# Kernel optimization log

Hardware: AMD Instinct MI355X
Metric: run time of the kernel (lower is better)

## Reference

```python
import jax, jax.numpy as jnp
import numpy as np

D_MODEL = 1024
N_HEADS = 16
D_K = D_MODEL // N_HEADS


def _glorot(key, fan_in, fan_out):
    limit = np.sqrt(6.0 / (fan_in + fan_out)).astype(np.float32)
    return jax.random.uniform(key, (fan_in, fan_out), jnp.float32, -limit, limit)


def setup_inputs() -> dict:
    key = jax.random.key(0)
    kx, kq, kk, kv = jax.random.split(key, 4)
    x = jax.random.normal(kx, (2, 2048, D_MODEL), jnp.float32)
    Wq = _glorot(kq, D_MODEL, D_MODEL)
    Wk = _glorot(kk, D_MODEL, D_MODEL)
    Wv = _glorot(kv, D_MODEL, D_MODEL)
    bq = jnp.zeros((D_MODEL,), jnp.float32)
    bk = jnp.zeros((D_MODEL,), jnp.float32)
    bv = jnp.zeros((D_MODEL,), jnp.float32)
    return {"x": x, "Wq": Wq, "bq": bq, "Wk": Wk, "bk": bk, "Wv": Wv, "bv": bv}


def reference(x, Wq, bq, Wk, bk, Wv, bv):
    B, S, _ = x.shape
    # QKV projections (Dense layers with bias)
    q = (x @ Wq + bq).reshape(B, S, N_HEADS, D_K).transpose(0, 2, 1, 3)  # [B,H,S,Dk]
    k = (x @ Wk + bk).reshape(B, S, N_HEADS, D_K).transpose(0, 2, 1, 3)
    v = (x @ Wv + bv).reshape(B, S, N_HEADS, D_K).transpose(0, 2, 1, 3)
    # raw exp-based softmax (NO max subtraction, per original module)
    scores = jnp.einsum('bhqd,bhkd->bhqk', q, k) / np.sqrt(D_K).astype(np.float32)
    scores = jnp.exp(scores)
    attn = scores / (jnp.sum(scores, axis=-1, keepdims=True) + 1e-8)
    context = jnp.einsum('bhqk,bhkd->bhqd', attn, v)  # [B,H,S,Dk]
    return context.transpose(0, 2, 1, 3).reshape(B, S, N_HEADS * D_K)
```

## Files before the change

### kernel.cpp

```cpp
#include <hip/hip_runtime.h>
#include <hip/hip_bf16.h>
#include <stdint.h>

typedef __bf16 bf16x8 __attribute__((ext_vector_type(8)));
typedef __bf16 bf16x4 __attribute__((ext_vector_type(4)));
typedef float  f32x4  __attribute__((ext_vector_type(4)));
typedef short  s16x4  __attribute__((ext_vector_type(4)));
typedef short  s16x8  __attribute__((ext_vector_type(8)));
typedef unsigned short u16_t;

#define MFMA(a, b, c)   __builtin_amdgcn_mfma_f32_16x16x32_bf16((a), (b), (c), 0, 0, 0)

__device__ __forceinline__ bf16x8 cat8(s16x4 a, s16x4 b) {
  s16x8 t = __builtin_shufflevector(a, b, 0, 1, 2, 3, 4, 5, 6, 7);
  return *(bf16x8*)&t;
}
__device__ __forceinline__ bf16x8 b8(s16x8 v) {
  bf16x8 r; __builtin_memcpy(&r, &v, 16); return r;
}

__device__ __forceinline__ void cp16(const void* g, void* l) {
  __builtin_amdgcn_global_load_lds(
      (const __attribute__((address_space(1))) unsigned int*)g,
      (__attribute__((address_space(3))) unsigned int*)l, 16, 0, 0);
}

__global__ __launch_bounds__(256) void k_prep(const float* __restrict__ x,
                                              const float* __restrict__ W0,
                                              const float* __restrict__ W1,
                                              const float* __restrict__ W2,
                                              u16_t* __restrict__ xb,
                                              u16_t* __restrict__ Wt) {
  __shared__ u16_t T[64][65];
  int bx = blockIdx.x, t = threadIdx.x;
  if (bx < 4096) {
    int i = bx * 256 + t;
    float4 f = ((const float4*)x)[i];
    bf16x4 o = {(__bf16)f.x, (__bf16)f.y, (__bf16)f.z, (__bf16)f.w};
    *(bf16x4*)&xb[(size_t)i * 4] = o;
    return;
  }
  int j = bx - 4096;
  int nx = j & 15, ny = (j >> 4) & 15, z = j >> 8;
  const float* W = z == 0 ? W0 : (z == 1 ? W1 : W2);
  int k0 = ny * 64, n0 = nx * 64;
#pragma unroll
  for (int i = 0; i < 16; i++) {
    int e = i * 256 + t, r = e >> 6, c = e & 63;
    __bf16 hv = (__bf16)W[(size_t)(k0 + r) * 1024 + n0 + c];
    T[r][c] = *(u16_t*)&hv;
  }
  __syncthreads();
  size_t base = ((size_t)z * 1024 + n0) * 1024 + k0;
#pragma unroll
  for (int i = 0; i < 16; i++) {
    int e = i * 256 + t, r = e >> 6, c = e & 63;
    Wt[base + (size_t)r * 1024 + c] = T[c][r];
  }
}

__global__ __launch_bounds__(512, 2) void k_gemm_qkv(
    const u16_t* __restrict__ A, const u16_t* __restrict__ Bt,
    const float* __restrict__ bq, const float* __restrict__ bk,
    const float* __restrict__ bv,
    u16_t* __restrict__ Qo, u16_t* __restrict__ Ko, u16_t* __restrict__ Vo) {
  __shared__ u16_t smem[57344];
  u16_t* As = smem;
  u16_t* Bs = smem + 32768;

  const int tid = threadIdx.x, lane = tid & 63, wv = tid >> 6;
  const int quad = lane >> 4, col = lane & 15;
  const int wm = wv >> 2, wn = wv & 3;

  int bid = blockIdx.x;
  int wg = (bid & 7) * 32 + (bid >> 3);
  const int tn = (wg & 15) * 192, tm = (wg >> 4) << 8;

  const int r16 = lane >> 2, c4 = lane & 3;
  const int srow = wv * 16 + r16;
  const int skoff = ((c4 ^ ((r16 >> 1) & 3)) << 3);
  const int sdst = srow * 32 + (c4 << 3);
  const size_t gA0 = (size_t)(tm + srow) * 1024 + skoff;
  const size_t gB0 = (size_t)(tn + srow) * 1024 + skoff;

  f32x4 acc[8][3] = {};

#define STAGE(kt, h, b) do {                                     \
    int dA_ = (b) * 16384 + (h) * 8192 + sdst;                   \
    int dB_ = (b) * 12288 + (h) * 6144 + sdst;                   \
    size_t s_ = (size_t)(kt) * 64 + (h) * 32;                    \
    cp16(A + gA0 + s_, As + dA_);                                \
    cp16(A + gA0 + s_ + (size_t)128 * 1024, As + dA_ + 4096);    \
    cp16(Bt + gB0 + s_, Bs + dB_);                               \
    if (wv < 4)                                                  \
      cp16(Bt + gB0 + s_ + (size_t)128 * 1024, Bs + dB_ + 4096); \
  } while (0)

#define BAR()    asm volatile("s_barrier" ::: "memory")
#define WAITV(N) asm volatile("s_waitcnt vmcnt(" #N ")" ::: "memory")
#define WAITL()  asm volatile("s_waitcnt lgkmcnt(0)" ::: "memory")
#define SCHED0() __builtin_amdgcn_sched_barrier(0)

  STAGE(0, 0, 0);
  STAGE(0, 1, 0);
  WAITV(3);
  BAR();

  const int swz8 = (((lane >> 4) ^ ((col >> 1) & 3)) << 3);
  const int abase = (wm * 128 + col) * 32 + swz8;
  const int bbase = (wn * 48 + col) * 32 + swz8;

  for (int t = 0; t < 16; ++t) {
    const int cur = t & 1, nxt = cur ^ 1;
    const u16_t* Ap = As + cur * 16384;
    const u16_t* Bp = Bs + cur * 12288;
    bf16x8 af[4], bf[3];

#pragma unroll
    for (int i = 0; i < 4; i++) af[i] = *(const bf16x8*)&Ap[abase + i * 512];
#pragma unroll
    for (int j = 0; j < 3; j++) bf[j] = *(const bf16x8*)&Bp[bbase + j * 512];
    if (t + 1 < 16) STAGE(t + 1, 0, nxt);
    BAR(); WAITL(); SCHED0();
    __builtin_amdgcn_s_setprio(1);
#pragma unroll
    for (int i = 0; i < 4; i++)
#pragma unroll
      for (int j = 0; j < 3; j++) acc[i][j] = MFMA(af[i], bf[j], acc[i][j]);
    __builtin_amdgcn_s_setprio(0);
    BAR();

#pragma unroll
    for (int i = 0; i < 4; i++) af[i] = *(const bf16x8*)&Ap[abase + (i + 4) * 512];
    if (t + 1 < 16) { STAGE(t + 1, 1, nxt); WAITV(6); }
    else            { WAITV(0); }
    BAR(); WAITL(); SCHED0();
    __builtin_amdgcn_s_setprio(1);
#pragma unroll
    for (int i = 0; i < 4; i++)
#pragma unroll
      for (int j = 0; j < 3; j++) acc[i + 4][j] = MFMA(af[i], bf[j], acc[i + 4][j]);
    __builtin_amdgcn_s_setprio(0);
    BAR();

#pragma unroll
    for (int i = 0; i < 4; i++) af[i] = *(const bf16x8*)&Ap[8192 + abase + i * 512];
#pragma unroll
    for (int j = 0; j < 3; j++) bf[j] = *(const bf16x8*)&Bp[6144 + bbase + j * 512];
    BAR(); WAITL(); SCHED0();
    __builtin_amdgcn_s_setprio(1);
#pragma unroll
    for (int i = 0; i < 4; i++)
#pragma unroll
      for (int j = 0; j < 3; j++) acc[i][j] = MFMA(af[i], bf[j], acc[i][j]);
    __builtin_amdgcn_s_setprio(0);
    BAR();

#pragma unroll
    for (int i = 0; i < 4; i++) af[i] = *(const bf16x8*)&Ap[8192 + abase + (i + 4) * 512];
    if (t + 1 < 16) WAITV(3);
    WAITL();
    BAR(); SCHED0();
    __builtin_amdgcn_s_setprio(1);
#pragma unroll
    for (int i = 0; i < 4; i++)
#pragma unroll
      for (int j = 0; j < 3; j++) acc[i + 4][j] = MFMA(af[i], bf[j], acc[i + 4][j]);
    __builtin_amdgcn_s_setprio(0);
    BAR();
  }

#undef STAGE

#pragma unroll
  for (int nt = 0; nt < 3; nt++) {
    int gn = tn + wn * 48 + nt * 16 + col;
    int mat = gn >> 10, d = gn & 1023, h = d >> 6, dk = d & 63;
    const float* bias = mat == 0 ? bq : (mat == 1 ? bk : bv);
    float bb = bias[d];
    if (mat == 2) {
#pragma unroll
      for (int mt = 0; mt < 8; mt++) {
        int gm = tm + wm * 128 + mt * 16 + quad * 4;
        int b = gm >> 11, s = gm & 2047;
        bf16x4 pk4;
#pragma unroll
        for (int r = 0; r < 4; r++) pk4[r] = (__bf16)(acc[mt][nt][r] + bb);
        *(bf16x4*)&Vo[((size_t)((b * 16 + h) * 64 + dk)) * 2048 + s] = pk4;
      }
    } else {
      u16_t* O = mat == 0 ? Qo : Ko;
      const float scl = mat == 0 ? 0.18033688011112042f : 1.0f;
#pragma unroll
      for (int mt = 0; mt < 8; mt++) {
#pragma unroll
        for (int r = 0; r < 4; r++) {
          int gm = tm + wm * 128 + mt * 16 + quad * 4 + r;
          int b = gm >> 11, s = gm & 2047;
          __bf16 hv = (__bf16)((acc[mt][nt][r] + bb) * scl);
          O[((size_t)((b * 16 + h) * 2048 + s)) * 64 + dk] = *(u16_t*)&hv;
        }
      }
    }
  }
}

__global__ __launch_bounds__(256, 2) void k_attn(const u16_t* __restrict__ Q,
                                                 const u16_t* __restrict__ K,
                                                 const u16_t* __restrict__ Vt,
                                                 float* __restrict__ out) {
  __shared__ u16_t smem[24576];
  u16_t* Qs  = smem;
  u16_t* Ksb = smem + 8192;
  u16_t* Vsb = smem + 16384;
  const int tid = threadIdx.x, lane = tid & 63, wv = tid >> 6;
  const int quad = lane >> 4, col = lane & 15;

  const int bid = blockIdx.x;
  const int bh = (bid & 7) + 8 * ((bid >> 3) >> 4);
  const int qt = (bid >> 3) & 15;
  const int b = bh >> 4, h = bh & 15;
  const int r8 = lane >> 3, c8 = lane & 7;

  const u16_t* Qg = Q + ((size_t)bh * 2048 + qt * 128) * 64;
  const u16_t* Kg = K + (size_t)bh * 2048 * 64;
  const u16_t* Vg = Vt + (size_t)bh * 64 * 2048;

  const int lch  = c8 ^ r8;
  const int row0 = (wv * 2) * 8 + r8, row1 = (wv * 2 + 1) * 8 + r8;
  const int ldst0 = (wv * 2) * 512 + lane * 8;
  const int ldst1 = (wv * 2 + 1) * 512 + lane * 8;
  const int gk0 = row0 * 64 + lch * 8,   gk1 = row1 * 64 + lch * 8;
  const int gv0 = row0 * 2048 + lch * 8, gv1 = row1 * 2048 + lch * 8;

#pragma unroll
  for (int i = 0; i < 4; i++) {
    int c = wv * 4 + i;
    cp16(Qg + (c * 8 + r8) * 64 + lch * 8, Qs + c * 512 + lane * 8);
  }
  cp16(Kg + gk0, Ksb + ldst0);
  cp16(Kg + gk1, Ksb + ldst1);
  __syncthreads();

  bf16x8 qf[2][2];
#pragma unroll
  for (int nt = 0; nt < 2; nt++)
#pragma unroll
    for (int ks = 0; ks < 2; ks++) {
      int row = wv * 32 + nt * 16 + col;
      qf[nt][ks] = *(const bf16x8*)&Qs[row * 64 + (((ks * 4 + quad) ^ (row & 7)) * 8)];
    }

  int ka[2][4];
#pragma unroll
  for (int ks = 0; ks < 2; ks++)
#pragma unroll
    for (int mt = 0; mt < 4; mt++) {
      int row = mt * 16 + col;
      ka[ks][mt] = row * 64 + (((ks * 4 + quad) ^ (row & 7)) * 8);
    }
  int va0[2][4], va1[2][4];
#pragma unroll
  for (int g = 0; g < 2; g++)
#pragma unroll
    for (int dt = 0; dt < 4; dt++) {
      int row = dt * 16 + col;
      int cc = g * 4 + (quad >> 1);
      va0[g][dt] = row * 64 + ((cc ^ (row & 7)) * 8) + (quad & 1) * 4;
      va1[g][dt] = row * 64 + (((cc + 2) ^ (row & 7)) * 8) + (quad & 1) * 4;
    }

  const short one_bf = (short)0x3F80;
  s16x8 ones8s = {one_bf, one_bf, one_bf, one_bf, one_bf, one_bf, one_bf, one_bf};
  const bf16x8 ones8 = *(bf16x8*)&ones8s;
  const f32x4 z4 = {0.f, 0.f, 0.f, 0.f};

  f32x4 ao[2][4] = {};
  f32x4 dn[2] = {};
  s16x8 pA[2][2] = {}, pB[2][2] = {};

#define ATTN_STEP(KT, CUR, PFW, PFR, DO_PV, DO_PRE) do {                              \
    const u16_t* Kc = Ksb + (CUR) * 4096;                                             \
    const u16_t* Vp = Vsb + ((CUR) ^ 1) * 4096;                                       \
    u16_t* Kn = Ksb + ((CUR) ^ 1) * 4096;                                             \
    u16_t* Vn = Vsb + (CUR) * 4096;                                                   \
    if (DO_PRE) {                                                                     \
      const u16_t* kb = Kg + (size_t)((KT) + 1) * 4096;                               \
      cp16(kb + gk0, Kn + ldst0);                                                     \
      cp16(kb + gk1, Kn + ldst1);                                                     \
    }                                                                                 \
    {                                                                                 \
      const u16_t* vb = Vg + (size_t)(KT) * 64;                                       \
      cp16(vb + gv0, Vn + ldst0);                                                     \
      cp16(vb + gv1, Vn + ldst1);                                                     \
    }                                                                                 \
    f32x4 sc[4][2];                                                                   \
    __builtin_amdgcn_s_setprio(1);                                                    \
    _Pragma("unroll")                                                                 \
    for (int ks = 0; ks < 2; ks++) {                                                  \
      bf16x8 kf[4];                                                                   \
      _Pragma("unroll")                                                               \
      for (int mt = 0; mt < 4; mt++) kf[mt] = *(const bf16x8*)&Kc[ka[ks][mt]];        \
      _Pragma("unroll")                                                               \
      for (int mt = 0; mt < 4; mt++)                                                  \
        _Pragma("unroll")                                                             \
        for (int nt = 0; nt < 2; nt++)                                                \
          sc[mt][nt] = ks ? MFMA(kf[mt], qf[nt][1], sc[mt][nt])                       \
                          : MFMA(kf[mt], qf[nt][0], z4);                              \
    }                                                                                 \
    if (DO_PV) {                                                                      \
      bf16x8 pa00 = b8(PFR[0][0]), pa01 = b8(PFR[0][1]);                              \
      bf16x8 pa10 = b8(PFR[1][0]), pa11 = b8(PFR[1][1]);                              \
      _Pragma("unroll")                                                               \
      for (int dt = 0; dt < 4; dt++) {                                                \
        bf16x8 vv0 = cat8(*(const s16x4*)&Vp[va0[0][dt]],                             \
                          *(const s16x4*)&Vp[va1[0][dt]]);                            \
        bf16x8 vv1 = cat8(*(const s16x4*)&Vp[va0[1][dt]],                             \
                          *(const s16x4*)&Vp[va1[1][dt]]);                            \
        ao[0][dt] = MFMA(pa00, vv0, ao[0][dt]);                                       \
        ao[0][dt] = MFMA(pa01, vv1, ao[0][dt]);                                       \
        ao[1][dt] = MFMA(pa10, vv0, ao[1][dt]);                                       \
        ao[1][dt] = MFMA(pa11, vv1, ao[1][dt]);                                       \
      }                                                                               \
    }                                                                                 \
    __builtin_amdgcn_s_setprio(0);                                                    \
    _Pragma("unroll")                                                                 \
    for (int mt = 0; mt < 4; mt++)                                                    \
      _Pragma("unroll")                                                               \
      for (int nt = 0; nt < 2; nt++)                                                  \
        _Pragma("unroll")                                                             \
        for (int r = 0; r < 4; r++) {                                                 \
          __bf16 e = (__bf16)__builtin_amdgcn_exp2f(sc[mt][nt][r]);                   \
          PFW[nt][mt >> 1][(mt & 1) * 4 + r] = *(short*)&e;                           \
        }                                                                             \
    dn[0] = MFMA(b8(PFW[0][0]), ones8, dn[0]);                                        \
    dn[0] = MFMA(b8(PFW[0][1]), ones8, dn[0]);                                        \
    dn[1] = MFMA(b8(PFW[1][0]), ones8, dn[1]);                                        \
    dn[1] = MFMA(b8(PFW[1][1]), ones8, dn[1]);                                        \
    __syncthreads();                                                                  \
  } while (0)

  ATTN_STEP(0, 0, pA, pB, 0, 1);
  ATTN_STEP(1, 1, pB, pA, 1, 1);
#pragma unroll 1
  for (int kt2 = 1; kt2 < 15; kt2++) {
    int kt0 = kt2 * 2;
    ATTN_STEP(kt0,     0, pA, pB, 1, 1);
    ATTN_STEP(kt0 + 1, 1, pB, pA, 1, 1);
  }
  ATTN_STEP(30, 0, pA, pB, 1, 1);
  ATTN_STEP(31, 1, pB, pA, 1, 0);
#undef ATTN_STEP

  {
    const u16_t* Vp = Vsb + 4096;
    bf16x8 pa00 = b8(pB[0][0]), pa01 = b8(pB[0][1]);
    bf16x8 pa10 = b8(pB[1][0]), pa11 = b8(pB[1][1]);
#pragma unroll
    for (int dt = 0; dt < 4; dt++) {
      bf16x8 vv0 = cat8(*(const s16x4*)&Vp[va0[0][dt]], *(const s16x4*)&Vp[va1[0][dt]]);
      bf16x8 vv1 = cat8(*(const s16x4*)&Vp[va0[1][dt]], *(const s16x4*)&Vp[va1[1][dt]]);
      ao[0][dt] = MFMA(pa00, vv0, ao[0][dt]);
      ao[0][dt] = MFMA(pa01, vv1, ao[0][dt]);
      ao[1][dt] = MFMA(pa10, vv0, ao[1][dt]);
      ao[1][dt] = MFMA(pa11, vv1, ao[1][dt]);
    }
  }

#pragma unroll
  for (int nt = 0; nt < 2; nt++) {
    float inv[4];
#pragma unroll
    for (int r = 0; r < 4; r++)
      inv[r] = 1.0f / (dn[nt][r] + 1e-8f);
#pragma unroll
    for (int dt = 0; dt < 4; dt++) {
#pragma unroll
      for (int r = 0; r < 4; r++) {
        float v = ao[nt][dt][r] * inv[r];
        int s = qt * 128 + wv * 32 + nt * 16 + quad * 4 + r;
        out[((size_t)b * 2048 + s) * 1024 + h * 64 + dt * 16 + col] = v;
      }
    }
  }
}

extern "C" void kernel_launch(void* const* d_in, const int* in_sizes, int n_in,
                              void* d_out, int out_size, void* d_ws, size_t ws_size,
                              hipStream_t stream) {
  const float* x  = (const float*)d_in[0];
  const float* Wq = (const float*)d_in[1];
  const float* bq = (const float*)d_in[2];
  const float* Wk = (const float*)d_in[3];
  const float* bk = (const float*)d_in[4];
  const float* Wv = (const float*)d_in[5];
  const float* bv = (const float*)d_in[6];
  float* out = (float*)d_out;

  char* ws = (char*)d_ws;
  u16_t* xb  = (u16_t*)(ws);
  u16_t* Wt  = (u16_t*)(ws + 8388608);
  u16_t* Qb  = (u16_t*)(ws + 14680064);
  u16_t* Kb  = (u16_t*)(ws + 23068672);
  u16_t* Vtb = (u16_t*)(ws + 31457280);

  hipLaunchKernelGGL(k_prep, dim3(4864), dim3(256), 0, stream, x, Wq, Wk, Wv, xb, Wt);
  hipLaunchKernelGGL(k_gemm_qkv, dim3(256), dim3(512), 0, stream,
                     xb, Wt, bq, bk, bv, Qb, Kb, Vtb);
  hipLaunchKernelGGL(k_attn, dim3(512), dim3(256), 0, stream, Qb, Kb, Vtb, out);
}
```

Measured before the change: 159.9 us.

## Double KV tile per pipeline step to halve barriers in attention kernel

Each pipeline step of the attention kernel now covers 128 keys as two 64-key sub-tiles instead of 64 keys, so there are 16 steps instead of 32. This halves the __syncthreads barriers and loop overhead per block and gives the scheduler more independent MFMA work between them. The exp conversion now sits inside the score loop at high priority, and the denominator MFMAs moved before the priority reset. In exchange, LDS use grows from 48KB to 80KB per block, which may limit occupancy under the 2-blocks-per-CU bound, and the doubled P-fragment arrays raise register pressure.

After: 157.0 us. No clear change (-1.9%).

```diff
diff --git a/kernel.cpp b/kernel.cpp
--- a/kernel.cpp
+++ b/kernel.cpp
@@ -209,10 +209,10 @@
                                                  const u16_t* __restrict__ K,
                                                  const u16_t* __restrict__ Vt,
                                                  float* __restrict__ out) {
-  __shared__ u16_t smem[24576];
+  __shared__ u16_t smem[40960];
   u16_t* Qs  = smem;
   u16_t* Ksb = smem + 8192;
-  u16_t* Vsb = smem + 16384;
+  u16_t* Vsb = smem + 24576;
   const int tid = threadIdx.x, lane = tid & 63, wv = tid >> 6;
   const int quad = lane >> 4, col = lane & 15;
 
@@ -240,6 +240,8 @@
   }
   cp16(Kg + gk0, Ksb + ldst0);
   cp16(Kg + gk1, Ksb + ldst1);
+  cp16(Kg + 4096 + gk0, Ksb + 4096 + ldst0);
+  cp16(Kg + 4096 + gk1, Ksb + 4096 + ldst1);
   __syncthreads();
 
   bf16x8 qf[2][2];
@@ -277,93 +279,110 @@
 
   f32x4 ao[2][4] = {};
   f32x4 dn[2] = {};
-  s16x8 pA[2][2] = {}, pB[2][2] = {};
+  s16x8 pA[2][2][2] = {}, pB[2][2][2] = {};
 
 #define ATTN_STEP(KT, CUR, PFW, PFR, DO_PV, DO_PRE) do {                              \
-    const u16_t* Kc = Ksb + (CUR) * 4096;                                             \
-    const u16_t* Vp = Vsb + ((CUR) ^ 1) * 4096;                                       \
-    u16_t* Kn = Ksb + ((CUR) ^ 1) * 4096;                                             \
-    u16_t* Vn = Vsb + (CUR) * 4096;                                                   \
+    const u16_t* Kc = Ksb + (CUR) * 8192;                                             \
+    const u16_t* Vp = Vsb + ((CUR) ^ 1) * 8192;                                       \
+    u16_t* Kn = Ksb + ((CUR) ^ 1) * 8192;                                             \
+    u16_t* Vn = Vsb + (CUR) * 8192;                                                   \
     if (DO_PRE) {                                                                     \
-      const u16_t* kb = Kg + (size_t)((KT) + 1) * 4096;                               \
+      const u16_t* kb = Kg + (size_t)((KT) + 1) * 8192;                               \
       cp16(kb + gk0, Kn + ldst0);                                                     \
       cp16(kb + gk1, Kn + ldst1);                                                     \
+      cp16(kb + 4096 + gk0, Kn + 4096 + ldst0);                                       \
+      cp16(kb + 4096 + gk1, Kn + 4096 + ldst1);                                       \
     }                                                                                 \
     {                                                                                 \
-      const u16_t* vb = Vg + (size_t)(KT) * 64;                                       \
+      const u16_t* vb = Vg + (size_t)(KT) * 128;                                      \
       cp16(vb + gv0, Vn + ldst0);                                                     \
       cp16(vb + gv1, Vn + ldst1);                                                     \
+      cp16(vb + 64 + gv0, Vn + 4096 + ldst0);                                         \
+      cp16(vb + 64 + gv1, Vn + 4096 + ldst1);                                         \
     }                                                                                 \
-    f32x4 sc[4][2];                                                                   \
     __builtin_amdgcn_s_setprio(1);                                                    \
     _Pragma("unroll")                                                                 \
-    for (int ks = 0; ks < 2; ks++) {                                                  \
-      bf16x8 kf[4];                                                                   \
+    for (int s = 0; s < 2; s++) {                                                     \
+      const u16_t* Ks_ = Kc + s * 4096;                                               \
+      f32x4 sc[4][2];                                                                 \
       _Pragma("unroll")                                                               \
-      for (int mt = 0; mt < 4; mt++) kf[mt] = *(const bf16x8*)&Kc[ka[ks][mt]];        \
+      for (int ks = 0; ks < 2; ks++) {                                                \
+        bf16x8 kf[4];                                                                 \
+        _Pragma("unroll")                                                             \
+        for (int mt = 0; mt < 4; mt++) kf[mt] = *(const bf16x8*)&Ks_[ka[ks][mt]];     \
+        _Pragma("unroll")                                                             \
+        for (int mt = 0; mt < 4; mt++)                                                \
+          _Pragma("unroll")                                                           \
+          for (int nt = 0; nt < 2; nt++)                                              \
+            sc[mt][nt] = ks ? MFMA(kf[mt], qf[nt][1], sc[mt][nt])                     \
+                            : MFMA(kf[mt], qf[nt][0], z4);                            \
+      }                                                                               \
       _Pragma("unroll")                                                               \
       for (int mt = 0; mt < 4; mt++)                                                  \
         _Pragma("unroll")                                                             \
         for (int nt = 0; nt < 2; nt++)                                                \
-          sc[mt][nt] = ks ? MFMA(kf[mt], qf[nt][1], sc[mt][nt])                       \
-                          : MFMA(kf[mt], qf[nt][0], z4);                              \
+          _Pragma("unroll")                                                           \
+          for (int r = 0; r < 4; r++) {                                               \
+            __bf16 e = (__bf16)__builtin_amdgcn_exp2f(sc[mt][nt][r]);                 \
+            PFW[s][nt][mt >> 1][(mt & 1) * 4 + r] = *(short*)&e;                      \
+          }                                                                           \
     }                                                                                 \
     if (DO_PV) {                                                                      \
-      bf16x8 pa00 = b8(PFR[0][0]), pa01 = b8(PFR[0][1]);                              \
-      bf16x8 pa10 = b8(PFR[1][0]), pa11 = b8(PFR[1][1]);                              \
       _Pragma("unroll")                                                               \
-      for (int dt = 0; dt < 4; dt++) {                                                \
-        bf16x8 vv0 = cat8(*(const s16x4*)&Vp[va0[0][dt]],                             \
-                          *(const s16x4*)&Vp[va1[0][dt]]);                            \
-        bf16x8 vv1 = cat8(*(const s16x4*)&Vp[va0[1][dt]],                             \
-                          *(const s16x4*)&Vp[va1[1][dt]]);                            \
-        ao[0][dt] = MFMA(pa00, vv0, ao[0][dt]);                                       \
-        ao[0][dt] = MFMA(pa01, vv1, ao[0][dt]);                                       \
-        ao[1][dt] = MFMA(pa10, vv0, ao[1][dt]);                                       \
-        ao[1][dt] = MFMA(pa11, vv1, ao[1][dt]);                                       \
+      for (int s = 0; s < 2; s++) {                                                   \
+        const u16_t* Vs_ = Vp + s * 4096;                                             \
+        bf16x8 pa00 = b8(PFR[s][0][0]), pa01 = b8(PFR[s][0][1]);                      \
+        bf16x8 pa10 = b8(PFR[s][1][0]), pa11 = b8(PFR[s][1][1]);                      \
+        _Pragma("unroll")                                                             \
+        for (int dt = 0; dt < 4; dt++) {                                              \
+          bf16x8 vv0 = cat8(*(const s16x4*)&Vs_[va0[0][dt]],                          \
+                            *(const s16x4*)&Vs_[va1[0][dt]]);                         \
+          bf16x8 vv1 = cat8(*(const s16x4*)&Vs_[va0[1][dt]],                          \
+                            *(const s16x4*)&Vs_[va1[1][dt]]);                         \
+          ao[0][dt] = MFMA(pa00, vv0, ao[0][dt]);                                     \
+          ao[0][dt] = MFMA(pa01, vv1, ao[0][dt]);                                     \
+          ao[1][dt] = MFMA(pa10, vv0, ao[1][dt]);                                     \
+          ao[1][dt] = MFMA(pa11, vv1, ao[1][dt]);                                     \
+        }                                                                             \
       }                                                                               \
     }                                                                                 \
+    _Pragma("unroll")                                                                 \
+    for (int s = 0; s < 2; s++) {                                                     \
+      dn[0] = MFMA(b8(PFW[s][0][0]), ones8, dn[0]);                                   \
+      dn[0] = MFMA(b8(PFW[s][0][1]), ones8, dn[0]);                                   \
+      dn[1] = MFMA(b8(PFW[s][1][0]), ones8, dn[1]);                                   \
+      dn[1] = MFMA(b8(PFW[s][1][1]), ones8, dn[1]);                                   \
+    }                                                                                 \
     __builtin_amdgcn_s_setprio(0);                                                    \
-    _Pragma("unroll")                                                                 \
-    for (int mt = 0; mt < 4; mt++)                                                    \
-      _Pragma("unroll")                                                               \
-      for (int nt = 0; nt < 2; nt++)                                                  \
-        _Pragma("unroll")                                                             \
-        for (int r = 0; r < 4; r++) {                                                 \
-          __bf16 e = (__bf16)__builtin_amdgcn_exp2f(sc[mt][nt][r]);                   \
-          PFW[nt][mt >> 1][(mt & 1) * 4 + r] = *(short*)&e;                           \
-        }                                                                             \
-    dn[0] = MFMA(b8(PFW[0][0]), ones8, dn[0]);                                        \
-    dn[0] = MFMA(b8(PFW[0][1]), ones8, dn[0]);                                        \
-    dn[1] = MFMA(b8(PFW[1][0]), ones8, dn[1]);                                        \
-    dn[1] = MFMA(b8(PFW[1][1]), ones8, dn[1]);                                        \
     __syncthreads();                                                                  \
   } while (0)
 
   ATTN_STEP(0, 0, pA, pB, 0, 1);
-  ATTN_STEP(1, 1, pB, pA, 1, 1);
 #pragma unroll 1
-  for (int kt2 = 1; kt2 < 15; kt2++) {
-    int kt0 = kt2 * 2;
-    ATTN_STEP(kt0,     0, pA, pB, 1, 1);
-    ATTN_STEP(kt0 + 1, 1, pB, pA, 1, 1);
-  }
-  ATTN_STEP(30, 0, pA, pB, 1, 1);
-  ATTN_STEP(31, 1, pB, pA, 1, 0);
+  for (int kt2 = 0; kt2 < 7; kt2++) {
+    int kt0 = kt2 * 2 + 1;
+    ATTN_STEP(kt0,     1, pB, pA, 1, 1);
+    ATTN_STEP(kt0 + 1, 0, pA, pB, 1, 1);
+  }
+  ATTN_STEP(15, 1, pB, pA, 1, 0);
 #undef ATTN_STEP
 
   {
-    const u16_t* Vp = Vsb + 4096;
-    bf16x8 pa00 = b8(pB[0][0]), pa01 = b8(pB[0][1]);
-    bf16x8 pa10 = b8(pB[1][0]), pa11 = b8(pB[1][1]);
-#pragma unroll
-    for (int dt = 0; dt < 4; dt++) {
-      bf16x8 vv0 = cat8(*(const s16x4*)&Vp[va0[0][dt]], *(const s16x4*)&Vp[va1[0][dt]]);
-      bf16x8 vv1 = cat8(*(const s16x4*)&Vp[va0[1][dt]], *(const s16x4*)&Vp[va1[1][dt]]);
-      ao[0][dt] = MFMA(pa00, vv0, ao[0][dt]);
-      ao[0][dt] = MFMA(pa01, vv1, ao[0][dt]);
-      ao[1][dt] = MFMA(pa10, vv0, ao[1][dt]);
-      ao[1][dt] = MFMA(pa11, vv1, ao[1][dt]);
+    const u16_t* Vp = Vsb + 8192;
+#pragma unroll
+    for (int s = 0; s < 2; s++) {
+      const u16_t* Vs_ = Vp + s * 4096;
+      bf16x8 pa00 = b8(pB[s][0][0]), pa01 = b8(pB[s][0][1]);
+      bf16x8 pa10 = b8(pB[s][1][0]), pa11 = b8(pB[s][1][1]);
+#pragma unroll
+      for (int dt = 0; dt < 4; dt++) {
+        bf16x8 vv0 = cat8(*(const s16x4*)&Vs_[va0[0][dt]], *(const s16x4*)&Vs_[va1[0][dt]]);
+        bf16x8 vv1 = cat8(*(const s16x4*)&Vs_[va0[1][dt]], *(const s16x4*)&Vs_[va1[1][dt]]);
+        ao[0][dt] = MFMA(pa00, vv0, ao[0][dt]);
+        ao[0][dt] = MFMA(pa01, vv1, ao[0][dt]);
+        ao[1][dt] = MFMA(pa10, vv0, ao[1][dt]);
+        ao[1][dt] = MFMA(pa11, vv1, ao[1][dt]);
+      }
     }
   }
 
```
